# Performance work log

Measured on AMD Instinct MI355X. Metric: run time of the kernel, lower is better.

The kernel has to match this reference:

```python
import jax, jax.numpy as jnp
from jax import lax
import numpy as np

SQRT2 = 1.4142135623730951
STYLE_DIM = 512
MOD_SCALE = 1.0 / np.sqrt(float(STYLE_DIM))          # EqualLinear modulation, lr_mul=1
MAP_SCALE = 0.01 / np.sqrt(float(STYLE_DIM))          # mapping EqualLinear, lr_mul=0.01
LR_MUL = 0.01


def _blur_kernel():
    k = np.array([1.0, 3.0, 3.0, 1.0], dtype=np.float32)
    k = k[None, :] * k[:, None]
    return jnp.asarray(k / k.sum())


def upfirdn2d(x, k, up=1, down=1, pad=(0, 0)):
    # torch upfirdn2d inserts (up-1) zeros AFTER each sample -> extra trailing pad of up-1
    C = x.shape[1]
    kern = jnp.tile(k[None, None], (C, 1, 1, 1))  # depthwise [C,1,kh,kw] (kernel symmetric, no flip needed)
    p = (pad[0], pad[1] + up - 1)
    return lax.conv_general_dilated(x, kern, (down, down), [p, p], lhs_dilation=(up, up),
                                    dimension_numbers=('NCHW', 'OIHW', 'NCHW'), feature_group_count=C)


def fused_lrelu(x, b):
    return jax.nn.leaky_relu(x + b.reshape(1, -1, 1, 1), 0.2) * SQRT2


def grouped_conv(x, w, pad, up):
    # x: [B,I,H,W], w: [B,O,I,k,k] per-sample weights -> grouped conv with B groups
    B, O, I, kh, kw = w.shape
    xg = x.reshape(1, B * I, x.shape[2], x.shape[3])
    if up:
        # torch conv_transpose2d(stride=2, padding=0) == dilated conv with spatially flipped kernel
        wf = jnp.flip(w, (-2, -1)).reshape(B * O, I, kh, kw)
        out = lax.conv_general_dilated(xg, wf, (1, 1), [(kh - 1, kh - 1), (kw - 1, kw - 1)],
                                       lhs_dilation=(2, 2),
                                       dimension_numbers=('NCHW', 'OIHW', 'NCHW'), feature_group_count=B)
    else:
        out = lax.conv_general_dilated(xg, w.reshape(B * O, I, kh, kw), (1, 1), [(pad, pad), (pad, pad)],
                                       dimension_numbers=('NCHW', 'OIHW', 'NCHW'), feature_group_count=B)
    return out.reshape(B, O, out.shape[2], out.shape[3])


def mod_conv(x, weight, style, mod_w, mod_b, demodulate, up, blur_k):
    # weight: [O,I,k,k]; style: [B,512]
    s = style @ (mod_w * MOD_SCALE).T + mod_b                       # [B,I]
    scale = 1.0 / np.sqrt(float(weight.shape[1] * weight.shape[2] * weight.shape[3]))
    w = scale * weight[None] * s[:, None, :, None, None]            # [B,O,I,k,k]
    if demodulate:
        d = lax.rsqrt(jnp.sum(w * w, axis=(2, 3, 4)) + 1e-8)
        w = w * d[:, :, None, None, None]
    out = grouped_conv(x, w, weight.shape[-1] // 2, up)
    if up:
        out = upfirdn2d(out, blur_k * 4.0, pad=(1, 1))              # Blur pad from p=len(k)-2-(3-1)=0
    return out


def _forward(z, mlp_w, mlp_b, const_input, conv_w, conv_mod_w, conv_mod_b, conv_bias,
             noise_strength, rgb_w, rgb_mod_w, rgb_mod_b, rgb_bias):
    B = z.shape[0]
    blur_k = _blur_kernel()
    w_lat = z * lax.rsqrt(jnp.mean(z * z, axis=1, keepdims=True) + 1e-8)
    for i in range(mlp_w.shape[0]):
        w_lat = jax.nn.leaky_relu(w_lat @ (mlp_w[i] * MAP_SCALE).T + mlp_b[i] * LR_MUL, 0.2) * SQRT2
    nkey = jax.random.key(7)

    def noise(l, shape):
        return jax.random.normal(jax.random.fold_in(nkey, l), (shape[0], 1, shape[2], shape[3]), dtype=jnp.float32)

    def styled(x, l, up):
        y = mod_conv(x, conv_w[l], w_lat, conv_mod_w[l], conv_mod_b[l], True, up, blur_k)
        y = y + noise_strength[l] * noise(l, y.shape)
        return fused_lrelu(y, conv_bias[l])

    def to_rgb(x, i):
        y = mod_conv(x, rgb_w[i], w_lat, rgb_mod_w[i], rgb_mod_b[i], False, False, blur_k)
        return y + rgb_bias[i].reshape(1, -1, 1, 1)

    out = jnp.tile(const_input, (B, 1, 1, 1))   # ConstantInput (shift=0 -> identity rolls)
    out = styled(out, 0, False)
    skip = to_rgb(out, 0)
    l = 1
    for blk in range(3):  # resolutions 8, 16, 32
        out = styled(out, l, True); l += 1
        out = styled(out, l, False); l += 1
        # Upsample(skip): kernel*factor^2, pad=(2,1), up=2
        skip = to_rgb(out, blk + 1) + upfirdn2d(skip, blur_k * 4.0, up=2, pad=(2, 1))
    return skip  # [B,3,32,32]


def setup_inputs() -> dict:
    key = jax.random.key(0)
    ks = jax.random.split(key, 8)
    B, S, C = 8, 512, 512
    return {
        'z': jax.random.normal(ks[0], (B, S), jnp.float32),
        'mlp_w': jax.random.normal(ks[1], (8, S, S), jnp.float32),
        'mlp_b': jnp.zeros((8, S), jnp.float32),
        'const_input': jax.random.normal(ks[2], (1, C, 4, 4), jnp.float32),
        'conv_w': jax.random.normal(ks[3], (7, C, C, 3, 3), jnp.float32),
        'conv_mod_w': jax.random.normal(ks[4], (7, C, S), jnp.float32),
        'conv_mod_b': jnp.ones((7, C), jnp.float32),
        'conv_bias': jnp.zeros((7, C), jnp.float32),
        'noise_strength': jax.random.normal(ks[5], (7,), jnp.float32) * 0.1,
        'rgb_w': jax.random.normal(ks[6], (4, 3, C, 1, 1), jnp.float32),
        'rgb_mod_w': jax.random.normal(ks[7], (4, C, S), jnp.float32),
        'rgb_mod_b': jnp.ones((4, C), jnp.float32),
        'rgb_bias': jnp.zeros((4, 3), jnp.float32),
    }


def reference(z, mlp_w, mlp_b, const_input, conv_w, conv_mod_w, conv_mod_b, conv_bias,
              noise_strength, rgb_w, rgb_mod_w, rgb_mod_b, rgb_bias):
    return _forward(z, mlp_w, mlp_b, const_input, conv_w, conv_mod_w, conv_mod_b, conv_bias,
                    noise_strength, rgb_w, rgb_mod_w, rgb_mod_b, rgb_bias)
```

## Files before the change

kernel.cpp:

```cpp
#include <hip/hip_runtime.h>


#define SQRT2F      1.41421356f
#define MAP_SCALE   4.41941738e-04f
#define MOD_SCALE   4.41941738e-02f
#define CONV_SCALE  1.47313913e-02f
#define RGB_SCALE   4.41941738e-02f

typedef __attribute__((ext_vector_type(8))) short bf16x8;
typedef __attribute__((ext_vector_type(16))) float f32x16;

__device__ __forceinline__ float bf2f(ushort u) {
    return __uint_as_float(((unsigned)u) << 16);
}
__device__ __forceinline__ ushort f2bf(float f) {
    unsigned u = __float_as_uint(f);
    unsigned r = (u + 0x7FFFu + ((u >> 16) & 1u)) >> 16;
    return (ushort)r;
}
__device__ __forceinline__ void store4bf(ushort* p, float a, float b, float c, float d) {
    union { ushort u[4]; uint2 v; } x;
    x.u[0] = f2bf(a); x.u[1] = f2bf(b); x.u[2] = f2bf(c); x.u[3] = f2bf(d);
    *(uint2*)p = x.v;
}

typedef __attribute__((address_space(1))) const unsigned int GAS;
typedef __attribute__((address_space(3))) unsigned int LAS;
__device__ __forceinline__ void gload_lds16(const ushort* g, ushort* l) {
    __builtin_amdgcn_global_load_lds((GAS*)g, (LAS*)l, 16, 0, 0);
}


__device__ __forceinline__ unsigned rotl32(unsigned x, int r) {
    return (x << r) | (x >> (32 - r));
}

__device__ void threefry2x32(unsigned k0, unsigned k1, unsigned x0, unsigned x1,
                             unsigned& o0, unsigned& o1) {
    unsigned k2 = k0 ^ k1 ^ 0x1BD11BDAu;
    x0 += k0; x1 += k1;
    x0 += x1; x1 = rotl32(x1,13); x1 ^= x0;
    x0 += x1; x1 = rotl32(x1,15); x1 ^= x0;
    x0 += x1; x1 = rotl32(x1,26); x1 ^= x0;
    x0 += x1; x1 = rotl32(x1, 6); x1 ^= x0;
    x0 += k1; x1 += k2 + 1u;
    x0 += x1; x1 = rotl32(x1,17); x1 ^= x0;
    x0 += x1; x1 = rotl32(x1,29); x1 ^= x0;
    x0 += x1; x1 = rotl32(x1,16); x1 ^= x0;
    x0 += x1; x1 = rotl32(x1,24); x1 ^= x0;
    x0 += k2; x1 += k0 + 2u;
    x0 += x1; x1 = rotl32(x1,13); x1 ^= x0;
    x0 += x1; x1 = rotl32(x1,15); x1 ^= x0;
    x0 += x1; x1 = rotl32(x1,26); x1 ^= x0;
    x0 += x1; x1 = rotl32(x1, 6); x1 ^= x0;
    x0 += k0; x1 += k1 + 3u;
    x0 += x1; x1 = rotl32(x1,17); x1 ^= x0;
    x0 += x1; x1 = rotl32(x1,29); x1 ^= x0;
    x0 += x1; x1 = rotl32(x1,16); x1 ^= x0;
    x0 += x1; x1 = rotl32(x1,24); x1 ^= x0;
    x0 += k1; x1 += k2 + 4u;
    x0 += x1; x1 = rotl32(x1,13); x1 ^= x0;
    x0 += x1; x1 = rotl32(x1,15); x1 ^= x0;
    x0 += x1; x1 = rotl32(x1,26); x1 ^= x0;
    x0 += x1; x1 = rotl32(x1, 6); x1 ^= x0;
    x0 += k2; x1 += k0 + 5u;
    o0 = x0; o1 = x1;
}

__device__ float bits_to_normal(unsigned bits) {
    unsigned m = (bits >> 9) | 0x3F800000u;
    float f = __uint_as_float(m) - 1.0f;
    const float lo = -0.99999994f;
    float u = f * 2.0f + lo;
    u = fmaxf(lo, u);
    float w = -log1pf(-u * u);
    float p;
    if (w < 5.0f) {
        w -= 2.5f;
        p = 2.81022636e-08f;
        p = fmaf(p, w, 3.43273939e-07f);
        p = fmaf(p, w, -3.5233877e-06f);
        p = fmaf(p, w, -4.39150654e-06f);
        p = fmaf(p, w, 0.00021858087f);
        p = fmaf(p, w, -0.00125372503f);
        p = fmaf(p, w, -0.00417768164f);
        p = fmaf(p, w, 0.246640727f);
        p = fmaf(p, w, 1.50140941f);
    } else {
        w = sqrtf(w) - 3.0f;
        p = -0.000200214257f;
        p = fmaf(p, w, 0.000100950558f);
        p = fmaf(p, w, 0.00134934322f);
        p = fmaf(p, w, -0.00367342844f);
        p = fmaf(p, w, 0.00573950773f);
        p = fmaf(p, w, -0.0076224613f);
        p = fmaf(p, w, 0.00943887047f);
        p = fmaf(p, w, 1.00167406f);
        p = fmaf(p, w, 2.83297682f);
    }
    return 1.41421354f * (p * u);
}

__global__ void noise_kernel(float* __restrict__ nbuf) {
    int g = blockIdx.x * 256 + threadIdx.x;
    if (g >= 21632) return;
    const int off[8] = {0, 128, 640, 1152, 3200, 5248, 13440, 21632};
    int l = 0;
    while (l < 6 && g >= off[l + 1]) l++;
    int i = g - off[l];
    unsigned k0, k1;
    threefry2x32(0u, 7u, 0u, (unsigned)l, k0, k1);
    unsigned b0, b1;
    threefry2x32(k0, k1, 0u, (unsigned)i, b0, b1);
    nbuf[g] = bits_to_normal(b0 ^ b1);
}


__global__ void pixelnorm_kernel(const float* __restrict__ z, float* __restrict__ out) {
    int b = blockIdx.x;
    int lane = threadIdx.x;
    float v[8];
    float s = 0.f;
    #pragma unroll
    for (int j = 0; j < 8; j++) {
        v[j] = z[b * 512 + lane + (j << 6)];
        s += v[j] * v[j];
    }
    #pragma unroll
    for (int off = 32; off > 0; off >>= 1) s += __shfl_xor(s, off, 64);
    float norm = rsqrtf(s * (1.f / 512.f) + 1e-8f);
    #pragma unroll
    for (int j = 0; j < 8; j++)
        out[b * 512 + lane + (j << 6)] = v[j] * norm;
}

__global__ void dot512_kernel(const float* __restrict__ win, const float* __restrict__ W,
                              const float* __restrict__ bias, float* __restrict__ out,
                              int total, float wscale, float bscale, int mode) {
    int gt = blockIdx.x * blockDim.x + threadIdx.x;
    int wv = gt >> 6;
    int lane = gt & 63;
    if (wv >= total) return;
    int l = wv >> 12;
    int r = wv & 4095;
    int b = r >> 9;
    int o = r & 511;
    const float* wrow = W + ((size_t)(l * 512 + o) << 9);
    const float* xrow = win + ((size_t)b << 9);
    float s = 0.f;
    #pragma unroll
    for (int j = 0; j < 8; j++) {
        int k = lane + (j << 6);
        s += wrow[k] * xrow[k];
    }
    #pragma unroll
    for (int off = 32; off > 0; off >>= 1) s += __shfl_xor(s, off, 64);
    if (lane == 0) {
        float v = s * wscale + bias[l * 512 + o] * bscale;
        if (mode) v = (v > 0.f ? v : 0.2f * v) * SQRT2F;
        out[wv] = v;
    }
}

__global__ void wbconv_all(const float* __restrict__ cw, ushort* __restrict__ wb7,
                           float* __restrict__ wsq7) {
    int gid = blockIdx.x * 256 + threadIdx.x;
    if (gid >= 7 * 262144) return;
    int l = gid >> 18;
    int idx = gid & 262143;
    int o = idx >> 9, i = idx & 511;
    int flip = (l == 1 || l == 3 || l == 5);
    const float* p = cw + (size_t)gid * 9;
    float w9[9];
    float s = 0.f;
    #pragma unroll
    for (int t = 0; t < 9; t++) { w9[t] = p[t]; s += w9[t] * w9[t]; }
    wsq7[gid] = s;
    ushort* wb = wb7 + (size_t)l * 2359296;
    int c = i >> 5, kv = (i >> 3) & 3, e = i & 7;
    #pragma unroll
    for (int t = 0; t < 9; t++) {
        int tsrc = flip ? (8 - t) : t;
        wb[(size_t)(((c * 9 + t) * 4 + kv) * 512 + o) * 8 + e] = f2bf(w9[tsrc]);
    }
}

__global__ void demod_all(const float* __restrict__ wsq7, const float* __restrict__ sc,
                          float* __restrict__ dm) {
    int gt = blockIdx.x * blockDim.x + threadIdx.x;
    int wv = gt >> 6;
    int lane = gt & 63;
    if (wv >= 7 * 4096) return;
    int l = wv >> 12, b = (wv >> 9) & 7, o = wv & 511;
    const float* wr = wsq7 + (size_t)l * 262144 + ((size_t)o << 9);
    const float* sr = sc + l * 4096 + (b << 9);
    float s = 0.f;
    #pragma unroll
    for (int j = 0; j < 8; j++) {
        int k = lane + (j << 6);
        float sv = sr[k];
        s += wr[k] * sv * sv;
    }
    #pragma unroll
    for (int off = 32; off > 0; off >>= 1) s += __shfl_xor(s, off, 64);
    if (lane == 0) dm[wv] = rsqrtf(s * (1.f / 4608.f) + 1e-8f);
}

__global__ void prep0_kernel(const float* __restrict__ cinp, const float* __restrict__ s0,
                             ushort* __restrict__ X0p) {
    int gid = blockIdx.x * 256 + threadIdx.x;
    if (gid >= 8 * 36 * 64) return;
    int grp = gid & 63;
    int r = gid >> 6;
    int b = r / 36, rc = r % 36, row = rc / 6, col = rc % 6;
    int y = row - 1, x = col - 1;
    union { ushort u[8]; bf16x8 v; } pk;
    if (y >= 0 && y < 4 && x >= 0 && x < 4) {
        #pragma unroll
        for (int k = 0; k < 8; k++) {
            int ch = grp * 8 + k;
            pk.u[k] = f2bf(cinp[ch * 16 + y * 4 + x] * s0[b * 512 + ch]);
        }
    } else {
        #pragma unroll
        for (int k = 0; k < 8; k++) pk.u[k] = 0;
    }
    *(bf16x8*)&X0p[((size_t)grp * 288 + r) * 8] = pk.v;
}

template <int S, int NTILE, int WROWS, int KS, bool WUP>
__global__ __launch_bounds__(256, 2) void conv_dense5(
    const ushort* __restrict__ Xp, const ushort* __restrict__ wb,
    const float* __restrict__ dm, const float* __restrict__ nz,
    const float* __restrict__ nstr, const float* __restrict__ bias,
    const float* __restrict__ snext,
    ushort* __restrict__ T, ushort* __restrict__ XU, float* __restrict__ Pp) {
    constexpr int SP = S + 2, P2 = S * S, N = 8 * P2;
    constexpr int PXT = 8 * SP * SP;
    constexpr int JCOLS = NTILE / 128;
    constexpr int NPX = WROWS * SP;
    constexpr int ASZ = 9 * 4 * 64 * 8;
    constexpr int BSZ = NPX * 32;
    constexpr int PAIR = ASZ + BSZ;
    constexpr int NBU = NPX * 4;
    constexpr int NBT = (NBU + 255) / 256;
    constexpr int ROWMAX = 8 * SP - 1;
    constexpr int CK = 16 / KS;
    constexpr int DB = (CK > 1) ? 2 : 1;
    constexpr int MINB = (NBU > 192) ? ((NBU - 192 + 255) / 256) : 0;
    constexpr int NMIN = 9 + MINB;
    __shared__ __align__(16) ushort lds[DB * PAIR];

    const int tid = threadIdx.x, lane = tid & 63, nw = tid >> 6;
    const int hf = lane >> 5, l31 = lane & 31;
    const int o0 = blockIdx.x * 64;
    const int n0 = blockIdx.y * NTILE;
    const int ks = blockIdx.z;
    const int R0 = (n0 / P2) * SP + (n0 % P2) / S;

    int pixbase[JCOLS], nj[JCOLS];
    #pragma unroll
    for (int j = 0; j < JCOLS; j++) {
        int n = n0 + nw * (NTILE / 4) + j * 32 + l31;
        nj[j] = n;
        int b = n / P2, r = n % P2;
        int y = r / S, x = r % S;
        pixbase[j] = (b * SP + y - R0) * SP + x;
    }
    f32x16 acc[JCOLS][2];
    #pragma unroll
    for (int j = 0; j < JCOLS; j++) { acc[j][0] = (f32x16)0.f; acc[j][1] = (f32x16)0.f; }

    int bgo[NBT];
    bool bgv[NBT];
    #pragma unroll
    for (int r = 0; r < NBT; r++) {
        int t = tid + 256 * r;
        bgv[r] = t < NBU;
        int tt = bgv[r] ? t : 0;
        int px = tt % NPX, kv = tt / NPX;
        int rr = px / SP, cc = px % SP;
        int Rc = R0 + rr; if (Rc > ROWMAX) Rc = ROWMAX;
        bgo[r] = (kv * PXT + Rc * SP + cc) * 8;
    }
    const int aoff = (nw * 512 + o0 + lane) * 8;

    auto stage = [&](int cgi, int buf) {
        ushort* dstA = &lds[buf * PAIR + nw * 512];
        ushort* dstB = &lds[buf * PAIR + ASZ + nw * 512];
        const ushort* asrc = wb + (size_t)cgi * 147456 + aoff;
        #pragma unroll
        for (int r = 0; r < 9; r++)
            gload_lds16(asrc + r * 16384, dstA + r * 2048);
        const ushort* bsrc = Xp + (size_t)cgi * (PXT * 32);
        #pragma unroll
        for (int r = 0; r < NBT; r++)
            if (bgv[r])
                gload_lds16(bsrc + bgo[r], dstB + r * 2048);
    };

    stage(ks * CK, 0);
    for (int c = 0; c < CK; c++) {
        const int cur = c & 1;
        if (c + 1 < CK) {
            stage(ks * CK + c + 1, cur ^ 1);
            asm volatile("s_waitcnt vmcnt(%0)" :: "i"(NMIN) : "memory");
        } else {
            asm volatile("s_waitcnt vmcnt(0)" ::: "memory");
        }
        __builtin_amdgcn_s_barrier();
        __builtin_amdgcn_sched_barrier(0);
        const int bo = cur * PAIR;
        #pragma unroll
        for (int t = 0; t < 9; t++) {
            const int dpx = (t / 3) * SP + (t % 3);
            #pragma unroll
            for (int s = 0; s < 2; s++) {
                const int kv = s * 2 + hf;
                bf16x8 a0 = *(const bf16x8*)&lds[bo + ((t * 4 + kv) * 64 + l31) * 8];
                bf16x8 a1 = *(const bf16x8*)&lds[bo + ((t * 4 + kv) * 64 + 32 + l31) * 8];
                #pragma unroll
                for (int j = 0; j < JCOLS; j++) {
                    bf16x8 bf = *(const bf16x8*)&lds[bo + ASZ + (kv * NPX + pixbase[j] + dpx) * 8];
                    acc[j][0] = __builtin_amdgcn_mfma_f32_32x32x16_bf16(a0, bf, acc[j][0], 0, 0, 0);
                    acc[j][1] = __builtin_amdgcn_mfma_f32_32x32x16_bf16(a1, bf, acc[j][1], 0, 0, 0);
                }
            }
        }
        __builtin_amdgcn_sched_barrier(0);
        __builtin_amdgcn_s_barrier();
    }

    if constexpr (KS > 1) {
        #pragma unroll
        for (int j = 0; j < JCOLS; j++) {
            float* pb = Pp + (((size_t)(ks * N + nj[j])) << 9) + o0;
            #pragma unroll
            for (int sub = 0; sub < 2; sub++) {
                #pragma unroll
                for (int rq = 0; rq < 4; rq++) {
                    float4 v = make_float4(acc[j][sub][rq * 4 + 0], acc[j][sub][rq * 4 + 1],
                                           acc[j][sub][rq * 4 + 2], acc[j][sub][rq * 4 + 3]);
                    *(float4*)&pb[sub * 32 + 4 * hf + 8 * rq] = v;
                }
            }
        }
        return;
    }
    float ns = nstr[0];
    #pragma unroll
    for (int j = 0; j < JCOLS; j++) {
        int n = nj[j], b = n / P2, r = n % P2;
        float nv = nz[b * P2 + r];
        int y = r / S, x = r % S;
        size_t tbase = (size_t)n << 9;
        int gpx = (b * SP + y + 1) * SP + x + 1;
        #pragma unroll
        for (int sub = 0; sub < 2; sub++) {
            #pragma unroll
            for (int rq = 0; rq < 4; rq++) {
                int o = o0 + sub * 32 + 4 * hf + 8 * rq;
                float4 d4 = *(const float4*)&dm[b * 512 + o];
                float4 b4 = *(const float4*)&bias[o];
                float vv[4];
                #pragma unroll
                for (int ri = 0; ri < 4; ri++) {
                    float v = acc[j][sub][rq * 4 + ri] * (&d4.x)[ri] * CONV_SCALE
                              + ns * nv + (&b4.x)[ri];
                    vv[ri] = (v > 0.f ? v : 0.2f * v) * SQRT2F;
                }
                store4bf(T + tbase + o, vv[0], vv[1], vv[2], vv[3]);
                if (WUP) {
                    float4 s4 = *(const float4*)&snext[b * 512 + o];
                    store4bf(XU + ((size_t)(o >> 3) * PXT + gpx) * 8 + (o & 7),
                             vv[0] * s4.x, vv[1] * s4.y, vv[2] * s4.z, vv[3] * s4.w);
                }
            }
        }
    }
}

template <int S, int KS, bool WUP>
__global__ void combine_dense(const float* __restrict__ Pp, const float* __restrict__ dm,
                              const float* __restrict__ nz, const float* __restrict__ nstr,
                              const float* __restrict__ bias, const float* __restrict__ snext,
                              ushort* __restrict__ T, ushort* __restrict__ XU) {
    constexpr int P2 = S * S, N = 8 * P2, SP = S + 2;
    constexpr int PXT = 8 * SP * SP;
    int gid = blockIdx.x * 256 + threadIdx.x;
    int n = gid >> 7, og = (gid & 127) << 2;
    float4 sm = make_float4(0.f, 0.f, 0.f, 0.f);
    #pragma unroll
    for (int k = 0; k < KS; k++) {
        float4 p = *(const float4*)&Pp[(((size_t)(k * N + n)) << 9) + og];
        sm.x += p.x; sm.y += p.y; sm.z += p.z; sm.w += p.w;
    }
    int b = n / P2, r = n % P2;
    float nsv = nstr[0] * nz[b * P2 + r];
    float4 d4 = *(const float4*)&dm[b * 512 + og];
    float4 b4 = *(const float4*)&bias[og];
    float vv[4];
    const float* sp = &sm.x;
    #pragma unroll
    for (int i = 0; i < 4; i++) {
        float v = sp[i] * (&d4.x)[i] * CONV_SCALE + nsv + (&b4.x)[i];
        vv[i] = (v > 0.f ? v : 0.2f * v) * SQRT2F;
    }
    store4bf(&T[((size_t)n << 9) + og], vv[0], vv[1], vv[2], vv[3]);
    if (WUP) {
        int y = r / S, x = r % S;
        int gpx = (b * SP + y + 1) * SP + x + 1;
        float4 s4 = *(const float4*)&snext[b * 512 + og];
        store4bf(&XU[((size_t)(og >> 3) * PXT + gpx) * 8 + (og & 7)],
                 vv[0] * s4.x, vv[1] * s4.y, vv[2] * s4.z, vv[3] * s4.w);
    }
}

template <int HIN, int NTILE, int WRW>
__global__ __launch_bounds__(256, 2) void conv_up5(
    const ushort* __restrict__ Xp, const ushort* __restrict__ wb,
    const float* __restrict__ dm, ushort* __restrict__ U) {
    constexpr int SPI = HIN + 2, SOUT = 2 * HIN + 1, SPO = SOUT + 2;
    constexpr int PXT = 8 * SPI * SPI;
    constexpr int PXTO = 8 * SPO * SPO;
    constexpr int JCOLS = NTILE / 128;
    constexpr int NPX = WRW * SPI;
    constexpr int ASZ = 4 * 4 * 64 * 8;
    constexpr int BSZ = NPX * 32;
    constexpr int PAIR = ASZ + BSZ;
    constexpr int NBU = NPX * 4;
    constexpr int NBT = (NBU + 255) / 256;
    constexpr int ROWMAX = 8 * SPI - 1;
    constexpr int MINB = (NBU > 192) ? ((NBU - 192 + 255) / 256) : 0;
    constexpr int NMIN = 4 + MINB;
    __shared__ __align__(16) ushort lds[2 * PAIR];

    const int py = blockIdx.z >> 1, pxp = blockIdx.z & 1;
    const int GY = py ? HIN : HIN + 1, GX = pxp ? HIN : HIN + 1;
    const int GG = GY * GX, NCLS = 8 * GG;
    const int NTY = py ? 1 : 2, NTX = pxp ? 1 : 2, NT = NTY * NTX;
    const int n0 = blockIdx.y * NTILE;
    if (n0 >= NCLS) return;

    int taplist[4], toffs[4];
    {
        int k = 0;
        #pragma unroll
        for (int a2 = 0; a2 < 2; a2++) {
            if (a2 >= NTY) break;
            int dy = py ? 1 : a2 * 2;
            #pragma unroll
            for (int c2 = 0; c2 < 2; c2++) {
                if (c2 >= NTX) break;
                int dx = pxp ? 1 : c2 * 2;
                taplist[k] = dy * 3 + dx;
                toffs[k] = ((dy + py) >> 1) * SPI + ((dx + pxp) >> 1);
                k++;
            }
        }
        for (; k < 4; k++) { taplist[k] = 0; toffs[k] = 0; }
    }

    const int tid = threadIdx.x, lane = tid & 63, nw = tid >> 6;
    const int hf = lane >> 5, l31 = lane & 31;
    const int o0 = blockIdx.x * 64;
    const int R0 = (n0 / GG) * SPI + (n0 % GG) / GX;

    int pixbase[JCOLS], bj[JCOLS], gyj[JCOLS], gxj[JCOLS];
    bool validj[JCOLS];
    #pragma unroll
    for (int j = 0; j < JCOLS; j++) {
        int n = n0 + nw * (NTILE / 4) + j * 32 + l31;
        validj[j] = n < NCLS;
        int nc = validj[j] ? n : (NCLS - 1);
        int b = nc / GG, rem = nc % GG;
        int gy = rem / GX, gx = rem % GX;
        bj[j] = b; gyj[j] = gy; gxj[j] = gx;
        pixbase[j] = (b * SPI + gy - R0) * SPI + gx;
    }
    f32x16 acc[JCOLS][2];
    #pragma unroll
    for (int j = 0; j < JCOLS; j++) { acc[j][0] = (f32x16)0.f; acc[j][1] = (f32x16)0.f; }

    int bgo[NBT];
    bool bgv[NBT];
    #pragma unroll
    for (int r = 0; r < NBT; r++) {
        int t = tid + 256 * r;
        bgv[r] = t < NBU;
        int tt = bgv[r] ? t : 0;
        int px = tt % NPX, kv = tt / NPX;
        int rr = px / SPI, cc = px % SPI;
        int Rc = R0 + rr; if (Rc > ROWMAX) Rc = ROWMAX;
        bgo[r] = (kv * PXT + Rc * SPI + cc) * 8;
    }
    const int aoff = (nw * 512 + o0 + lane) * 8;
    int atap[4];
    #pragma unroll
    for (int r = 0; r < 4; r++) atap[r] = taplist[r] * 16384;

    auto stage = [&](int cgi, int buf) {
        ushort* dstA = &lds[buf * PAIR + nw * 512];
        ushort* dstB = &lds[buf * PAIR + ASZ + nw * 512];
        const ushort* asrc = wb + (size_t)cgi * 147456 + aoff;
        #pragma unroll
        for (int r = 0; r < 4; r++)
            gload_lds16(asrc + atap[r], dstA + r * 2048);
        const ushort* bsrc = Xp + (size_t)cgi * (PXT * 32);
        #pragma unroll
        for (int r = 0; r < NBT; r++)
            if (bgv[r])
                gload_lds16(bsrc + bgo[r], dstB + r * 2048);
    };

    stage(0, 0);
    for (int c = 0; c < 16; c++) {
        const int cur = c & 1;
        if (c + 1 < 16) {
            stage(c + 1, cur ^ 1);
            asm volatile("s_waitcnt vmcnt(%0)" :: "i"(NMIN) : "memory");
        } else {
            asm volatile("s_waitcnt vmcnt(0)" ::: "memory");
        }
        __builtin_amdgcn_s_barrier();
        __builtin_amdgcn_sched_barrier(0);
        const int bo = cur * PAIR;
        for (int tt = 0; tt < NT; ++tt) {
            const int dpx = toffs[tt];
            #pragma unroll
            for (int s = 0; s < 2; s++) {
                const int kv = s * 2 + hf;
                bf16x8 a0 = *(const bf16x8*)&lds[bo + ((tt * 4 + kv) * 64 + l31) * 8];
                bf16x8 a1 = *(const bf16x8*)&lds[bo + ((tt * 4 + kv) * 64 + 32 + l31) * 8];
                #pragma unroll
                for (int j = 0; j < JCOLS; j++) {
                    bf16x8 bf = *(const bf16x8*)&lds[bo + ASZ + (kv * NPX + pixbase[j] + dpx) * 8];
                    acc[j][0] = __builtin_amdgcn_mfma_f32_32x32x16_bf16(a0, bf, acc[j][0], 0, 0, 0);
                    acc[j][1] = __builtin_amdgcn_mfma_f32_32x32x16_bf16(a1, bf, acc[j][1], 0, 0, 0);
                }
            }
        }
        __builtin_amdgcn_sched_barrier(0);
        __builtin_amdgcn_s_barrier();
    }
    #pragma unroll
    for (int j = 0; j < JCOLS; j++) {
        if (!validj[j]) continue;
        int b = bj[j];
        int y = 2 * gyj[j] + py, x = 2 * gxj[j] + pxp;
        int gpx = (b * SPO + y + 1) * SPO + x + 1;
        #pragma unroll
        for (int sub = 0; sub < 2; sub++) {
            #pragma unroll
            for (int rq = 0; rq < 4; rq++) {
                int o = o0 + sub * 32 + 4 * hf + 8 * rq;
                float4 d4 = *(const float4*)&dm[b * 512 + o];
                float vv[4];
                #pragma unroll
                for (int ri = 0; ri < 4; ri++)
                    vv[ri] = acc[j][sub][rq * 4 + ri] * (&d4.x)[ri] * CONV_SCALE;
                store4bf(U + ((size_t)(o >> 3) * PXTO + gpx) * 8 + (o & 7),
                         vv[0], vv[1], vv[2], vv[3]);
            }
        }
    }
}

template <int SIN>
__global__ void blur_px(const ushort* __restrict__ U, const float* __restrict__ nz,
                        const float* __restrict__ nstr, const float* __restrict__ bias,
                        const float* __restrict__ snext, ushort* __restrict__ X) {
    constexpr int O = SIN - 1, SPI = SIN + 2, SPO = O + 2;
    constexpr int PXTU = 8 * SPI * SPI;
    constexpr int PXTO = 8 * SPO * SPO;
    int gid = blockIdx.x * 256 + threadIdx.x;
    if (gid >= 8 * O * O * 64) return;
    int grp = gid & 63;
    int pxl = gid >> 6;
    int b = pxl / (O * O), r = pxl % (O * O), u = r / O, vcol = r % O;
    const float k1[4] = {0.25f, 0.75f, 0.75f, 0.25f};
    float acc[8];
    #pragma unroll
    for (int k = 0; k < 8; k++) acc[k] = 0.f;
    const ushort* Ug = U + (size_t)grp * PXTU * 8;
    #pragma unroll
    for (int a = 0; a < 4; a++) {
        int row = b * SPI + u + a;
        #pragma unroll
        for (int c = 0; c < 4; c++) {
            float w = k1[a] * k1[c];
            bf16x8 v = *(const bf16x8*)&Ug[(size_t)(row * SPI + vcol + c) * 8];
            #pragma unroll
            for (int k = 0; k < 8; k++) acc[k] += w * bf2f((ushort)v[k]);
        }
    }
    float nsv = nstr[0] * nz[b * O * O + r];
    float4 b0 = *(const float4*)&bias[grp * 8];
    float4 b1 = *(const float4*)&bias[grp * 8 + 4];
    float4 s0 = *(const float4*)&snext[b * 512 + grp * 8];
    float4 s1 = *(const float4*)&snext[b * 512 + grp * 8 + 4];
    union { ushort us[8]; bf16x8 v; } pk;
    #pragma unroll
    for (int k = 0; k < 8; k++) {
        float bk = (k < 4) ? (&b0.x)[k] : (&b1.x)[k - 4];
        float sk = (k < 4) ? (&s0.x)[k] : (&s1.x)[k - 4];
        float v = acc[k] + nsv + bk;
        v = (v > 0.f ? v : 0.2f * v) * SQRT2F;
        pk.us[k] = f2bf(v * sk);
    }
    *(bf16x8*)&X[((size_t)grp * PXTO + (b * SPO + u + 1) * SPO + vcol + 1) * 8] = pk.v;
}

template <int H>
__global__ void skipup_kernel(const float* __restrict__ skip, float* __restrict__ out) {
    constexpr int O = 2 * H;
    int idx = blockIdx.x * 256 + threadIdx.x;
    if (idx >= 8 * 3 * O * O) return;
    int px = idx % (O * O);
    int bc = idx / (O * O);
    int u = px / O, v = px % O;
    const float k1[4] = {0.25f, 0.75f, 0.75f, 0.25f};
    const float* src = skip + (size_t)bc * (H * H);
    float acc = 0.f;
    #pragma unroll
    for (int ty = 0; ty < 4; ty++) {
        int r = u + ty - 2;
        if (r < 0 || (r & 1) || (r >> 1) >= H) continue;
        float rsum = 0.f;
        #pragma unroll
        for (int tx = 0; tx < 4; tx++) {
            int cc = v + tx - 2;
            if (cc < 0 || (cc & 1) || (cc >> 1) >= H) continue;
            rsum += k1[tx] * src[(r >> 1) * H + (cc >> 1)];
        }
        acc += k1[ty] * rsum;
    }
    out[(size_t)bc * (O * O) + px] = acc;
}

__global__ void torgb_px(const ushort* __restrict__ T, int P2,
                         const float* __restrict__ rgbw, const float* __restrict__ srgb,
                         const float* __restrict__ rbias, const float* __restrict__ skipup,
                         float* __restrict__ dst) {
    int b = blockIdx.x;
    int px = blockIdx.y * 4 + (threadIdx.x >> 6);
    int lane = threadIdx.x & 63;
    int c8 = lane * 8;
    bf16x8 v = *(const bf16x8*)&T[(((size_t)b * P2 + px) << 9) + c8];
    float4 sa = *(const float4*)&srgb[b * 512 + c8];
    float4 sb = *(const float4*)&srgb[b * 512 + c8 + 4];
    float xs[8];
    #pragma unroll
    for (int k = 0; k < 8; k++) {
        float sk = (k < 4) ? (&sa.x)[k] : (&sb.x)[k - 4];
        xs[k] = bf2f((ushort)v[k]) * sk;
    }
    float sums[3];
    #pragma unroll
    for (int c = 0; c < 3; c++) {
        float4 w0 = *(const float4*)&rgbw[c * 512 + c8];
        float4 w1 = *(const float4*)&rgbw[c * 512 + c8 + 4];
        float s = 0.f;
        #pragma unroll
        for (int k = 0; k < 8; k++) {
            float wk = (k < 4) ? (&w0.x)[k] : (&w1.x)[k - 4];
            s += xs[k] * wk;
        }
        #pragma unroll
        for (int off = 32; off > 0; off >>= 1) s += __shfl_xor(s, off, 64);
        sums[c] = s;
    }
    if (lane == 0) {
        #pragma unroll
        for (int c = 0; c < 3; c++) {
            float o = sums[c] * RGB_SCALE + rbias[c];
            if (skipup) o += skipup[((size_t)b * 3 + c) * P2 + px];
            dst[((size_t)b * 3 + c) * P2 + px] = o;
        }
    }
}


extern "C" void kernel_launch(void* const* d_in, const int* in_sizes, int n_in,
                              void* d_out, int out_size, void* d_ws, size_t ws_size,
                              hipStream_t stream) {
    const float* z      = (const float*)d_in[0];
    const float* mlp_w  = (const float*)d_in[1];
    const float* mlp_b  = (const float*)d_in[2];
    const float* cinp   = (const float*)d_in[3];
    const float* conv_w = (const float*)d_in[4];
    const float* cmw    = (const float*)d_in[5];
    const float* cmb    = (const float*)d_in[6];
    const float* cbias  = (const float*)d_in[7];
    const float* nstr   = (const float*)d_in[8];
    const float* rgbw   = (const float*)d_in[9];
    const float* rmw    = (const float*)d_in[10];
    const float* rmb    = (const float*)d_in[11];
    const float* rbias  = (const float*)d_in[12];
    float* out = (float*)d_out;
    float* ws = (float*)d_ws;

    float* wlatA = ws;
    float* wlatB = ws + 4096;
    float* sconv = ws + 8192;
    float* srgb  = ws + 36864;
    float* dem   = ws + 53248;
    float* noise = ws + 81920;
    float* skipA = ws + 103552;
    float* skipB = ws + 128128;
    float* skipU = ws + 152704;
    float* wsq7  = ws + 177280;
    ushort* wbuf7 = (ushort*)(ws + 2012288);
    float* Ppart = ws + 10269824;
    ushort* A1 = (ushort*)(ws + 12366976);
    ushort* A2 = (ushort*)(ws + 14875776);
    ushort* A3 = (ushort*)(ws + 17243264);

    ushort* X0p = A1;
    ushort* T0  = A2;
    ushort* XU1 = A3;
    ushort* U1  = A1;
    ushort* X2  = A2;
    ushort* T2  = A3;
    ushort* XU3 = A1;
    ushort* U3  = A2;
    ushort* X4  = A1;
    ushort* T4  = A2;
    ushort* XU5 = A3;
    ushort* U5  = A1;
    ushort* X6  = A2;
    ushort* T6  = A3;

    const size_t LWB = 2359296;

    wbconv_all<<<7168, 256, 0, stream>>>(conv_w, wbuf7, wsq7);
    noise_kernel<<<85, 256, 0, stream>>>(noise);

    pixelnorm_kernel<<<8, 64, 0, stream>>>(z, wlatA);
    float* a = wlatA;
    float* bb = wlatB;
    for (int i = 0; i < 8; i++) {
        dot512_kernel<<<1024, 256, 0, stream>>>(a, mlp_w + (size_t)i * 262144,
                                                mlp_b + i * 512, bb, 4096,
                                                MAP_SCALE, 0.01f, 1);
        float* t = a; a = bb; bb = t;
    }
    dot512_kernel<<<7168, 256, 0, stream>>>(a, cmw, cmb, sconv, 7 * 4096, MOD_SCALE, 1.0f, 0);
    dot512_kernel<<<4096, 256, 0, stream>>>(a, rmw, rmb, srgb, 4 * 4096, MOD_SCALE, 1.0f, 0);
    demod_all<<<7168, 256, 0, stream>>>(wsq7, sconv, dem);
    prep0_kernel<<<72, 256, 0, stream>>>(cinp, sconv, X0p);

    conv_dense5<4, 128, 48, 16, false><<<dim3(8, 1, 16), 256, 0, stream>>>(
        X0p, wbuf7, nullptr, nullptr, nullptr, nullptr, nullptr,
        nullptr, nullptr, Ppart);
    hipMemsetAsync(XU1, 0, (size_t)8 * 36 * 512 * 2, stream);
    combine_dense<4, 16, true><<<64, 256, 0, stream>>>(
        Ppart, dem, noise, nstr, cbias, sconv + 4096, T0, XU1);
    torgb_px<<<dim3(8, 4), 256, 0, stream>>>(T0, 16, rgbw, srgb, rbias, nullptr, skipA);

    hipMemsetAsync(U1, 0, (size_t)8 * 121 * 512 * 2, stream);
    conv_up5<4, 128, 48><<<dim3(8, 2, 4), 256, 0, stream>>>(XU1, wbuf7 + LWB, dem + 4096, U1);
    hipMemsetAsync(X2, 0, (size_t)8 * 100 * 512 * 2, stream);
    blur_px<9><<<128, 256, 0, stream>>>(U1, noise + 128, nstr + 1, cbias + 512,
                                        sconv + 2 * 4096, X2);

    conv_dense5<8, 128, 20, 8, false><<<dim3(8, 4, 8), 256, 0, stream>>>(
        X2, wbuf7 + 2 * LWB, nullptr, nullptr, nullptr, nullptr, nullptr,
        nullptr, nullptr, Ppart);
    hipMemsetAsync(XU3, 0, (size_t)8 * 100 * 512 * 2, stream);
    combine_dense<8, 8, true><<<256, 256, 0, stream>>>(
        Ppart, dem + 2 * 4096, noise + 640, nstr + 2, cbias + 2 * 512,
        sconv + 3 * 4096, T2, XU3);
    skipup_kernel<4><<<6, 256, 0, stream>>>(skipA, skipU);
    torgb_px<<<dim3(8, 16), 256, 0, stream>>>(T2, 64, rgbw + 1536, srgb + 4096,
                                              rbias + 3, skipU, skipB);

    hipMemsetAsync(U3, 0, (size_t)8 * 361 * 512 * 2, stream);
    conv_up5<8, 128, 22><<<dim3(8, 6, 4), 256, 0, stream>>>(XU3, wbuf7 + 3 * LWB,
                                                            dem + 3 * 4096, U3);
    hipMemsetAsync(X4, 0, (size_t)8 * 324 * 512 * 2, stream);
    blur_px<17><<<512, 256, 0, stream>>>(U3, noise + 1152, nstr + 3, cbias + 3 * 512,
                                         sconv + 4 * 4096, X4);

    conv_dense5<16, 128, 10, 2, false><<<dim3(8, 16, 2), 256, 0, stream>>>(
        X4, wbuf7 + 4 * LWB, nullptr, nullptr, nullptr, nullptr, nullptr,
        nullptr, nullptr, Ppart);
    hipMemsetAsync(XU5, 0, (size_t)8 * 324 * 512 * 2, stream);
    combine_dense<16, 2, true><<<1024, 256, 0, stream>>>(
        Ppart, dem + 4 * 4096, noise + 3200, nstr + 4, cbias + 4 * 512,
        sconv + 5 * 4096, T4, XU5);
    skipup_kernel<8><<<24, 256, 0, stream>>>(skipB, skipU);
    torgb_px<<<dim3(8, 64), 256, 0, stream>>>(T4, 256, rgbw + 2 * 1536, srgb + 2 * 4096,
                                              rbias + 6, skipU, skipA);

    hipMemsetAsync(U5, 0, (size_t)8 * 1225 * 512 * 2, stream);
    conv_up5<16, 256, 20><<<dim3(8, 10, 4), 256, 0, stream>>>(XU5, wbuf7 + 5 * LWB,
                                                              dem + 5 * 4096, U5);
    hipMemsetAsync(X6, 0, (size_t)8 * 1156 * 512 * 2, stream);
    blur_px<33><<<2048, 256, 0, stream>>>(U5, noise + 5248, nstr + 5, cbias + 5 * 512,
                                          sconv + 6 * 4096, X6);

    conv_dense5<32, 256, 10, 1, false><<<dim3(8, 32, 1), 256, 0, stream>>>(
        X6, wbuf7 + 6 * LWB, dem + 6 * 4096, noise + 13440, nstr + 6, cbias + 6 * 512,
        nullptr, T6, nullptr, nullptr);
    skipup_kernel<16><<<96, 256, 0, stream>>>(skipA, skipU);
    torgb_px<<<dim3(8, 256), 256, 0, stream>>>(T6, 1024, rgbw + 3 * 1536, srgb + 3 * 4096,
                                               rbias + 9, skipU, out);
}
```

Baseline: 427.6 us.

## Split conv K across two wave groups with LDS reduction; tile weight-prep transpose

The dense conv kernel now runs 512 threads per block. Two groups of four waves each handle half of the kv channel slices and then combine their accumulators through an LDS reduction, which shortens each wave's MFMA chain and adds latency hiding within a block. The weight preprocessing kernel now stages a 64x32x9 weight tile in shared memory, so global reads are coalesced float4 loads and the bf16 weights are written as packed 16-byte stores instead of scattered 2-byte stores. The costs are a reduction pass with an extra barrier, one block per CU under the new launch bounds, and larger LDS use.

```diff
diff --git a/kernel.cpp b/kernel.cpp
--- a/kernel.cpp
+++ b/kernel.cpp
@@ -162,26 +162,55 @@
     }
 }
 
-__global__ void wbconv_all(const float* __restrict__ cw, ushort* __restrict__ wb7,
-                           float* __restrict__ wsq7) {
-    int gid = blockIdx.x * 256 + threadIdx.x;
-    if (gid >= 7 * 262144) return;
-    int l = gid >> 18;
-    int idx = gid & 262143;
-    int o = idx >> 9, i = idx & 511;
-    int flip = (l == 1 || l == 3 || l == 5);
-    const float* p = cw + (size_t)gid * 9;
-    float w9[9];
-    float s = 0.f;
-    #pragma unroll
-    for (int t = 0; t < 9; t++) { w9[t] = p[t]; s += w9[t] * w9[t]; }
-    wsq7[gid] = s;
+__global__ __launch_bounds__(256) void wbconv_all(const float* __restrict__ cw,
+                                                  ushort* __restrict__ wb7,
+                                                  float* __restrict__ wsq7) {
+    __shared__ float lg[288 * 65];
+    const int bid = blockIdx.x;
+    const int l = bid >> 7, rem = bid & 127, c = rem >> 3, og = rem & 7;
+    const int o0 = og * 64;
+    const int ibase = c * 32;
+    const int tid = threadIdx.x;
+    const int flip = (l == 1 || l == 3 || l == 5);
+
+    #pragma unroll
+    for (int r = 0; r < 18; r++) {
+        int u = tid + 256 * r;
+        int o = u / 72, w = u % 72;
+        const float* src = cw + ((size_t)((l * 512 + o0 + o) * 512 + ibase)) * 9 + w * 4;
+        float4 v = *(const float4*)src;
+        lg[(w * 4 + 0) * 65 + o] = v.x;
+        lg[(w * 4 + 1) * 65 + o] = v.y;
+        lg[(w * 4 + 2) * 65 + o] = v.z;
+        lg[(w * 4 + 3) * 65 + o] = v.w;
+    }
+    __syncthreads();
+
+    #pragma unroll
+    for (int r = 0; r < 8; r++) {
+        int u = tid + 256 * r;
+        int o = u >> 5, il = u & 31;
+        float s = 0.f;
+        #pragma unroll
+        for (int t = 0; t < 9; t++) {
+            float x = lg[(il * 9 + t) * 65 + o];
+            s += x * x;
+        }
+        wsq7[((size_t)(l * 512 + o0 + o)) * 512 + ibase + il] = s;
+    }
+
     ushort* wb = wb7 + (size_t)l * 2359296;
-    int c = i >> 5, kv = (i >> 3) & 3, e = i & 7;
-    #pragma unroll
-    for (int t = 0; t < 9; t++) {
+    #pragma unroll
+    for (int r = 0; r < 9; r++) {
+        int u = tid + 256 * r;
+        int o = u & 63, tk = u >> 6;
+        int t = tk >> 2, kv = tk & 3;
         int tsrc = flip ? (8 - t) : t;
-        wb[(size_t)(((c * 9 + t) * 4 + kv) * 512 + o) * 8 + e] = f2bf(w9[tsrc]);
+        union { ushort us[8]; uint4 v; } pk;
+        #pragma unroll
+        for (int e = 0; e < 8; e++)
+            pk.us[e] = f2bf(lg[((kv * 8 + e) * 9 + tsrc) * 65 + o]);
+        *(uint4*)&wb[(size_t)(((c * 9 + t) * 4 + kv) * 512 + o0 + o) * 8] = pk.v;
     }
 }
 
@@ -229,7 +258,7 @@
 }
 
 template <int S, int NTILE, int WROWS, int KS, bool WUP>
-__global__ __launch_bounds__(256, 2) void conv_dense5(
+__global__ __launch_bounds__(512, 1) void conv_dense6(
     const ushort* __restrict__ Xp, const ushort* __restrict__ wb,
     const float* __restrict__ dm, const float* __restrict__ nz,
     const float* __restrict__ nstr, const float* __restrict__ bias,
@@ -242,26 +271,33 @@
     constexpr int ASZ = 9 * 4 * 64 * 8;
     constexpr int BSZ = NPX * 32;
     constexpr int PAIR = ASZ + BSZ;
+    constexpr int NAU = 2304;
+    constexpr int NAT = 5;
     constexpr int NBU = NPX * 4;
-    constexpr int NBT = (NBU + 255) / 256;
+    constexpr int NBT = (NBU + 511) / 512;
     constexpr int ROWMAX = 8 * SP - 1;
     constexpr int CK = 16 / KS;
     constexpr int DB = (CK > 1) ? 2 : 1;
-    constexpr int MINB = (NBU > 192) ? ((NBU - 192 + 255) / 256) : 0;
-    constexpr int NMIN = 9 + MINB;
-    __shared__ __align__(16) ushort lds[DB * PAIR];
+    constexpr int NAF = 4;
+    constexpr int NBF = NBU / 512;
+    constexpr int NMIN = NAF + NBF;
+    constexpr int REDU = JCOLS * 16384;
+    constexpr int LDSZ = (DB * PAIR > REDU) ? DB * PAIR : REDU;
+    __shared__ __align__(16) ushort lds[LDSZ];
 
     const int tid = threadIdx.x, lane = tid & 63, nw = tid >> 6;
+    const int sw = nw >> 2, nww = nw & 3;
     const int hf = lane >> 5, l31 = lane & 31;
     const int o0 = blockIdx.x * 64;
     const int n0 = blockIdx.y * NTILE;
     const int ks = blockIdx.z;
     const int R0 = (n0 / P2) * SP + (n0 % P2) / S;
+    const int kvw = sw * 2 + hf;
 
     int pixbase[JCOLS], nj[JCOLS];
     #pragma unroll
     for (int j = 0; j < JCOLS; j++) {
-        int n = n0 + nw * (NTILE / 4) + j * 32 + l31;
+        int n = n0 + nww * (NTILE / 4) + j * 32 + l31;
         nj[j] = n;
         int b = n / P2, r = n % P2;
         int y = r / S, x = r % S;
@@ -275,7 +311,7 @@
     bool bgv[NBT];
     #pragma unroll
     for (int r = 0; r < NBT; r++) {
-        int t = tid + 256 * r;
+        int t = tid + 512 * r;
         bgv[r] = t < NBU;
         int tt = bgv[r] ? t : 0;
         int px = tt % NPX, kv = tt / NPX;
@@ -283,20 +319,24 @@
         int Rc = R0 + rr; if (Rc > ROWMAX) Rc = ROWMAX;
         bgo[r] = (kv * PXT + Rc * SP + cc) * 8;
     }
-    const int aoff = (nw * 512 + o0 + lane) * 8;
 
     auto stage = [&](int cgi, int buf) {
-        ushort* dstA = &lds[buf * PAIR + nw * 512];
-        ushort* dstB = &lds[buf * PAIR + ASZ + nw * 512];
-        const ushort* asrc = wb + (size_t)cgi * 147456 + aoff;
-        #pragma unroll
-        for (int r = 0; r < 9; r++)
-            gload_lds16(asrc + r * 16384, dstA + r * 2048);
+        ushort* base = &lds[buf * PAIR];
+        const ushort* asrc = wb + (size_t)cgi * 147456;
+        #pragma unroll
+        for (int r = 0; r < NAT; r++) {
+            int u = tid + 512 * r;
+            if (u < NAU) {
+                int row = u >> 6;
+                gload_lds16(asrc + ((size_t)(row * 512 + o0) + (u & 63)) * 8,
+                            base + (r * 512 + nw * 64) * 8);
+            }
+        }
         const ushort* bsrc = Xp + (size_t)cgi * (PXT * 32);
         #pragma unroll
         for (int r = 0; r < NBT; r++)
             if (bgv[r])
-                gload_lds16(bsrc + bgo[r], dstB + r * 2048);
+                gload_lds16(bsrc + bgo[r], base + ASZ + (r * 512 + nw * 64) * 8);
     };
 
     stage(ks * CK, 0);
@@ -314,22 +354,46 @@
         #pragma unroll
         for (int t = 0; t < 9; t++) {
             const int dpx = (t / 3) * SP + (t % 3);
+            bf16x8 a0 = *(const bf16x8*)&lds[bo + ((t * 4 + kvw) * 64 + l31) * 8];
+            bf16x8 a1 = *(const bf16x8*)&lds[bo + ((t * 4 + kvw) * 64 + 32 + l31) * 8];
             #pragma unroll
-            for (int s = 0; s < 2; s++) {
-                const int kv = s * 2 + hf;
-                bf16x8 a0 = *(const bf16x8*)&lds[bo + ((t * 4 + kv) * 64 + l31) * 8];
-                bf16x8 a1 = *(const bf16x8*)&lds[bo + ((t * 4 + kv) * 64 + 32 + l31) * 8];
-                #pragma unroll
-                for (int j = 0; j < JCOLS; j++) {
-                    bf16x8 bf = *(const bf16x8*)&lds[bo + ASZ + (kv * NPX + pixbase[j] + dpx) * 8];
-                    acc[j][0] = __builtin_amdgcn_mfma_f32_32x32x16_bf16(a0, bf, acc[j][0], 0, 0, 0);
-                    acc[j][1] = __builtin_amdgcn_mfma_f32_32x32x16_bf16(a1, bf, acc[j][1], 0, 0, 0);
-                }
+            for (int j = 0; j < JCOLS; j++) {
+                bf16x8 bf = *(const bf16x8*)&lds[bo + ASZ + (kvw * NPX + pixbase[j] + dpx) * 8];
+                acc[j][0] = __builtin_amdgcn_mfma_f32_32x32x16_bf16(a0, bf, acc[j][0], 0, 0, 0);
+                acc[j][1] = __builtin_amdgcn_mfma_f32_32x32x16_bf16(a1, bf, acc[j][1], 0, 0, 0);
             }
         }
         __builtin_amdgcn_sched_barrier(0);
         __builtin_amdgcn_s_barrier();
     }
+
+    #pragma unroll
+    for (int j = 0; j < JCOLS; j++)
+        #pragma unroll
+        for (int sub = 0; sub < 2; sub++)
+            #pragma unroll
+            for (int rq = 0; rq < 4; rq++)
+                if (sw == 1) {
+                    int sidx = (j * 2 + sub) * 4 + rq;
+                    float4 v = make_float4(acc[j][sub][rq * 4 + 0], acc[j][sub][rq * 4 + 1],
+                                           acc[j][sub][rq * 4 + 2], acc[j][sub][rq * 4 + 3]);
+                    *(float4*)&lds[sidx * 2048 + (nww * 64 + lane) * 8] = v;
+                }
+    __syncthreads();
+    if (sw == 1) return;
+    #pragma unroll
+    for (int j = 0; j < JCOLS; j++)
+        #pragma unroll
+        for (int sub = 0; sub < 2; sub++)
+            #pragma unroll
+            for (int rq = 0; rq < 4; rq++) {
+                int sidx = (j * 2 + sub) * 4 + rq;
+                float4 p = *(const float4*)&lds[sidx * 2048 + (nww * 64 + lane) * 8];
+                acc[j][sub][rq * 4 + 0] += p.x;
+                acc[j][sub][rq * 4 + 1] += p.y;
+                acc[j][sub][rq * 4 + 2] += p.z;
+                acc[j][sub][rq * 4 + 3] += p.w;
+            }
 
     if constexpr (KS > 1) {
         #pragma unroll
@@ -733,7 +797,7 @@
 
     const size_t LWB = 2359296;
 
-    wbconv_all<<<7168, 256, 0, stream>>>(conv_w, wbuf7, wsq7);
+    wbconv_all<<<896, 256, 0, stream>>>(conv_w, wbuf7, wsq7);
     noise_kernel<<<85, 256, 0, stream>>>(noise);
 
     pixelnorm_kernel<<<8, 64, 0, stream>>>(z, wlatA);
@@ -750,7 +814,7 @@
     demod_all<<<7168, 256, 0, stream>>>(wsq7, sconv, dem);
     prep0_kernel<<<72, 256, 0, stream>>>(cinp, sconv, X0p);
 
-    conv_dense5<4, 128, 48, 16, false><<<dim3(8, 1, 16), 256, 0, stream>>>(
+    conv_dense6<4, 128, 48, 16, false><<<dim3(8, 1, 16), 512, 0, stream>>>(
         X0p, wbuf7, nullptr, nullptr, nullptr, nullptr, nullptr,
         nullptr, nullptr, Ppart);
     hipMemsetAsync(XU1, 0, (size_t)8 * 36 * 512 * 2, stream);
@@ -764,7 +828,7 @@
     blur_px<9><<<128, 256, 0, stream>>>(U1, noise + 128, nstr + 1, cbias + 512,
                                         sconv + 2 * 4096, X2);
 
-    conv_dense5<8, 128, 20, 8, false><<<dim3(8, 4, 8), 256, 0, stream>>>(
+    conv_dense6<8, 128, 20, 8, false><<<dim3(8, 4, 8), 512, 0, stream>>>(
         X2, wbuf7 + 2 * LWB, nullptr, nullptr, nullptr, nullptr, nullptr,
         nullptr, nullptr, Ppart);
     hipMemsetAsync(XU3, 0, (size_t)8 * 100 * 512 * 2, stream);
@@ -782,7 +846,7 @@
     blur_px<17><<<512, 256, 0, stream>>>(U3, noise + 1152, nstr + 3, cbias + 3 * 512,
                                          sconv + 4 * 4096, X4);
 
-    conv_dense5<16, 128, 10, 2, false><<<dim3(8, 16, 2), 256, 0, stream>>>(
+    conv_dense6<16, 128, 10, 2, false><<<dim3(8, 16, 2), 512, 0, stream>>>(
         X4, wbuf7 + 4 * LWB, nullptr, nullptr, nullptr, nullptr, nullptr,
         nullptr, nullptr, Ppart);
     hipMemsetAsync(XU5, 0, (size_t)8 * 324 * 512 * 2, stream);
@@ -800,7 +864,7 @@
     blur_px<33><<<2048, 256, 0, stream>>>(U5, noise + 5248, nstr + 5, cbias + 5 * 512,
                                           sconv + 6 * 4096, X6);
 
-    conv_dense5<32, 256, 10, 1, false><<<dim3(8, 32, 1), 256, 0, stream>>>(
+    conv_dense6<32, 256, 10, 1, false><<<dim3(8, 32, 1), 512, 0, stream>>>(
         X6, wbuf7 + 6 * LWB, dem + 6 * 4096, noise + 13440, nstr + 6, cbias + 6 * 512,
         nullptr, T6, nullptr, nullptr);
     skipup_kernel<16><<<96, 256, 0, stream>>>(skipA, skipU);
```

Result: faster. 404.0 us (-5.5%).
